# Kernel optimization log

Hardware: AMD Instinct MI355X
Metric: run time of the kernel (lower is better)

Reference implementation:

```python
import jax, jax.numpy as jnp
import numpy as np

B, T, D = 8, 1024, 1024
L = 512          # quantizer_latent_dim
V = 8192         # codebook_size
COMMIT = 0.25
PERP_COEF = 0.1


def _l2norm(v, axis=-1):
    return v * jax.lax.rsqrt(jnp.sum(v * v, axis=axis, keepdims=True) + 1e-12)


def _sq_dist(a, b):
    # ||a||^2 - 2 a.b + ||b||^2, a:[N,L] b:[V,L] -> [N,V]
    a2 = jnp.sum(a * a, axis=1, keepdims=True)
    b2 = jnp.sum(b * b, axis=1)[None, :]
    return a2 - 2.0 * jnp.einsum('nl,vl->nv', a, b) + b2


def setup_inputs() -> dict:
    key = jax.random.key(0)
    ks = jax.random.split(key, 4)
    x = jax.random.normal(ks[0], (B, T, D), dtype=jnp.float32)
    codebook = jax.random.normal(ks[1], (V, D), dtype=jnp.float32)
    W_in = jax.random.normal(ks[2], (D, L), dtype=jnp.float32) * (1.0 / np.sqrt(D))
    b_in = jnp.zeros((L,), dtype=jnp.float32)
    W_code = jax.random.normal(ks[3], (D, L), dtype=jnp.float32) * (1.0 / np.sqrt(D))
    b_code = jnp.zeros((L,), dtype=jnp.float32)
    return {"x": x, "codebook": codebook, "W_in": W_in, "b_in": b_in,
            "W_code": W_code, "b_code": b_code}


def _train_loss(quantized, x):
    e_latent = jnp.mean((jax.lax.stop_gradient(quantized) - x) ** 2) * COMMIT
    q_latent = jnp.mean((quantized - jax.lax.stop_gradient(x)) ** 2)
    return e_latent + q_latent


def reference(x, codebook, W_in, b_in, W_code, b_code):
    xf = x.reshape(-1, D)                                      # [N, D]
    latent_input = _l2norm(xf @ W_in + b_in)                   # [N, L]
    latent_code = _l2norm(codebook @ W_code + b_code)          # [V, L]
    sg_latent_code = jax.lax.stop_gradient(_l2norm(latent_code))
    distances = _sq_dist(latent_input, sg_latent_code).reshape(B, T, V)

    # approx_min_k with aggregate_to_topk (k = top_k_value = 1)
    idx = jax.lax.approx_min_k(distances, k=1, reduction_dimension=-1,
                               aggregate_to_topk=True)[1][..., 0]   # [B, T]
    encodings = jax.nn.one_hot(idx, V, dtype=x.dtype)          # [B, T, V]
    quantized = jnp.einsum('btv,vd->btd', encodings, codebook) # [B, T, D]

    codebook_usage = jnp.sum(jnp.sum(encodings, axis=(0, 1)) > 0) / V

    # train=True path: stop-grad quantized, straight-through estimator
    q_sg = jax.lax.stop_gradient(quantized)
    loss = _train_loss(q_sg, x)
    latent_quantized = q_sg @ W_code + b_code                  # code_to_latent(quantized)
    latent_x = x @ W_in + b_in                                 # input_to_latent(x)
    loss = loss + _train_loss(latent_quantized, latent_x)

    quantized_st = x + jax.lax.stop_gradient(q_sg - x)

    avg_probs = jnp.mean(encodings.reshape(-1, V), axis=0)
    log_perplexity = -jnp.sum(avg_probs * jnp.log(avg_probs + 1e-10))
    perplexity = jnp.exp(log_perplexity)
    loss = loss + PERP_COEF * log_perplexity

    return quantized_st, loss, perplexity, codebook_usage
```

## Files before the change

kernel.cpp:

```cpp
#include <hip/hip_runtime.h>
#include <hip/hip_bf16.h>
#include <stdint.h>

#define NTOK 8192
#define DDIM 1024
#define LDIM 512
#define VCB  8192
#define MROWS 16384

typedef unsigned long long u64;
typedef unsigned short ushort_t;
typedef unsigned char u8;
typedef float f32x4 __attribute__((ext_vector_type(4)));
typedef short s16x8 __attribute__((ext_vector_type(8)));

#define OFF_AB     0ull
#define OFF_QB     0ull
#define OFF_P      ((u64)MROWS * DDIM * 2)
#define OFF_QF     (OFF_P + (u64)MROWS * LDIM * 2)
#define OFF_WT     (OFF_QF + (u64)MROWS * 512)
#define OFF_B2     (OFF_WT + (u64)2 * LDIM * DDIM * 2)
#define OFF_B2B    (OFF_B2 + (u64)VCB * 4)
#define OFF_PART   (OFF_B2B + (u64)VCB * 4)
#define OFF_HIST   (OFF_PART + (u64)NTOK * 64 * 4)
#define OFF_PARTQ  (OFF_HIST + (u64)VCB * 4)
#define OFF_PARTL  (OFF_PARTQ + (u64)NTOK * 4)

__device__ __forceinline__ unsigned key_of(float f) {
  unsigned u = __float_as_uint(f);
  return (u & 0x80000000u) ? ~u : (u | 0x80000000u);
}

__device__ __forceinline__ ushort_t f2bf(float f) {
  unsigned u = __float_as_uint(f);
  unsigned r = (u + 0x7fffu + ((u >> 16) & 1u)) >> 16;
  return (ushort_t)r;
}
__device__ __forceinline__ float bf2f(unsigned b) {
  return __uint_as_float(b << 16);
}
__device__ __forceinline__ unsigned pkbf(float a, float b) {
  __hip_bfloat162 h = __float22bfloat162_rn(make_float2(a, b));
  unsigned r;
  __builtin_memcpy(&r, &h, 4);
  return r;
}

__device__ __forceinline__ void gload_lds16(const void* g, void* l) {
  __builtin_amdgcn_global_load_lds(
      (const __attribute__((address_space(1))) unsigned int*)g,
      (__attribute__((address_space(3))) unsigned int*)l, 16, 0, 0);
}

__device__ __forceinline__ f32x4 mfma16(s16x8 a, s16x8 b, f32x4 c) {
  return __builtin_amdgcn_mfma_f32_16x16x32_bf16(a, b, c, 0, 0, 0);
}
__device__ __forceinline__ f32x4 mfma8(u64 a, u64 b, f32x4 c) {
  return __builtin_amdgcn_mfma_f32_16x16x32_fp8_fp8((long long)a, (long long)b,
                                                    c, 0, 0, 0);
}

__global__ __launch_bounds__(256)
void k_wt(const float* __restrict__ Wi, const float* __restrict__ Wc,
          ushort_t* __restrict__ Wt, int* __restrict__ hist) {
  __shared__ float tile[32][33];
  const int tx = threadIdx.x, ty = threadIdx.y;
  const int t = ty * 32 + tx;
  const int lb = blockIdx.z * 512 + blockIdx.y * 32 + blockIdx.x;
  if (lb < 32) hist[lb * 256 + t] = 0;
  const float* W = blockIdx.z ? Wc : Wi;
  ushort_t* O = Wt + (blockIdx.z ? (size_t)LDIM * DDIM : 0);
  const int k0 = blockIdx.x * 32, n0 = blockIdx.y * 32;
#pragma unroll
  for (int i = 0; i < 4; ++i)
    tile[ty * 4 + i][tx] = W[(size_t)(k0 + ty * 4 + i) * LDIM + n0 + tx];
  __syncthreads();
#pragma unroll
  for (int i = 0; i < 4; ++i)
    O[(size_t)(n0 + ty * 4 + i) * DDIM + k0 + tx] = f2bf(tile[tx][ty * 4 + i]);
}

__global__ __launch_bounds__(256)
void k_cast(const float* __restrict__ x, const float* __restrict__ cb,
            ushort_t* __restrict__ Ab) {
  size_t i = ((size_t)blockIdx.x * 256 + threadIdx.x) * 8;
  const size_t half = (size_t)NTOK * DDIM;
  const float* src = (i < half) ? (x + i) : (cb + (i - half));
  float4 a = *(const float4*)src;
  float4 b = *(const float4*)(src + 4);
  uint4 o = make_uint4(pkbf(a.x, a.y), pkbf(a.z, a.w),
                       pkbf(b.x, b.y), pkbf(b.z, b.w));
  *(uint4*)&Ab[i] = o;
}

__global__ __launch_bounds__(256)
void k_latent(const ushort_t* __restrict__ Ab, const ushort_t* __restrict__ Wt,
              const float* __restrict__ bi, const float* __restrict__ bc,
              ushort_t* __restrict__ Pb) {
  __shared__ __align__(16) ushort_t As[128 * 32];
  __shared__ __align__(16) ushort_t Bs[128 * 32];
  const int t = threadIdx.x;
  const int wave = t >> 6, lane = t & 63;
  const int col0 = blockIdx.x * 128;
  const int m0 = blockIdx.y * 128;
  const bool isCode = (m0 >= NTOK);
  const u8* A = (const u8*)(Ab + (size_t)m0 * DDIM);
  const u8* W = (const u8*)(Wt + (isCode ? (size_t)LDIM * DDIM : 0) +
                            (size_t)col0 * DDIM);
  const float* bias = isCode ? bc : bi;

  const int srow = lane >> 2;
  const int rA = wave * 16 + srow;
  const int rB = 64 + wave * 16 + srow;
  const size_t goA = (size_t)rA * 2048 +
                     (((lane & 3) ^ (rA & 3) ^ ((rA >> 2) & 3)) << 4);
  const size_t goB = (size_t)rB * 2048 +
                     (((lane & 3) ^ (rB & 3) ^ ((rB >> 2) & 3)) << 4);
  u8* lwA0 = (u8*)As + (wave * 16) * 64;
  u8* lwA1 = (u8*)As + (64 + wave * 16) * 64;
  u8* lwB0 = (u8*)Bs + (wave * 16) * 64;
  u8* lwB1 = (u8*)Bs + (64 + wave * 16) * 64;

  const int wm = wave >> 1, wn = wave & 1;
  const int m = lane & 15, q = lane >> 4;
  const int pq = (q ^ (m & 3) ^ ((m >> 2) & 3)) * 16;
  int roffA[4], roffB[4];
#pragma unroll
  for (int i = 0; i < 4; ++i) {
    roffA[i] = (wm * 64 + i * 16 + m) * 64 + pq;
    roffB[i] = (wn * 64 + i * 16 + m) * 64 + pq;
  }

  f32x4 acc[4][4];
#pragma unroll
  for (int i = 0; i < 4; ++i)
#pragma unroll
    for (int j = 0; j < 4; ++j) acc[i][j] = (f32x4)(0.f);

  for (int it = 0; it < DDIM / 32; ++it) {
    const size_t kb = (size_t)it * 64;
    __syncthreads();
    gload_lds16(A + goA + kb, lwA0);
    gload_lds16(A + goB + kb, lwA1);
    gload_lds16(W + goA + kb, lwB0);
    gload_lds16(W + goB + kb, lwB1);
    __syncthreads();
    s16x8 af[4], bfr[4];
#pragma unroll
    for (int i = 0; i < 4; ++i)
      af[i] = *(const s16x8*)((const u8*)As + roffA[i]);
#pragma unroll
    for (int j = 0; j < 4; ++j)
      bfr[j] = *(const s16x8*)((const u8*)Bs + roffB[j]);
#pragma unroll
    for (int i = 0; i < 4; ++i)
#pragma unroll
      for (int j = 0; j < 4; ++j)
        acc[i][j] = mfma16(af[i], bfr[j], acc[i][j]);
  }

  float bv[4];
#pragma unroll
  for (int j = 0; j < 4; ++j) bv[j] = bias[col0 + wn * 64 + j * 16 + m];
#pragma unroll
  for (int i = 0; i < 4; ++i)
#pragma unroll
    for (int j = 0; j < 4; ++j) {
      int col = col0 + wn * 64 + j * 16 + m;
#pragma unroll
      for (int reg = 0; reg < 4; ++reg) {
        int row = m0 + wm * 64 + i * 16 + q * 4 + reg;
        Pb[(size_t)row * LDIM + col] = f2bf(acc[i][j][reg] + bv[j]);
      }
    }
}

__global__ __launch_bounds__(256)
void k_rownorm(const ushort_t* __restrict__ P, u8* __restrict__ Qf,
               ushort_t* __restrict__ Qb, float* __restrict__ b2,
               float* __restrict__ b2b) {
  const int row = blockIdx.x;
  const int t = threadIdx.x;
  const int lane = t & 63, wid = t >> 6;
  __shared__ float red[4];
  __shared__ float2 red2[4];
  __shared__ float bcast;
  const int c = t >> 5;
  const int w = (2 * t) & 63;
  const int g = w >> 4, h = w & 15;
  const int k = c * 64 + ((h < 8) ? (g * 8 + h) : (32 + g * 8 + (h - 8)));
  unsigned pv = *(const unsigned*)&P[(size_t)row * LDIM + k];
  float v0 = bf2f(pv & 0xffffu), v1 = bf2f(pv >> 16);
  float s = fmaf(v0, v0, v1 * v1);
#pragma unroll
  for (int o = 32; o > 0; o >>= 1) s += __shfl_down(s, o, 64);
  if (lane == 0) red[wid] = s;
  __syncthreads();
  if (t == 0) {
    float tot = red[0] + red[1] + red[2] + red[3];
    bcast = (float)(1.0 / sqrt((double)tot + 1e-12));
  }
  __syncthreads();
  float rs = bcast;
  int p8 = __builtin_amdgcn_cvt_pk_fp8_f32(v0 * rs, v1 * rs, 0, false);
  ((ushort_t*)Qf)[(size_t)row * 256 + t] = (ushort_t)((unsigned)p8 & 0xFFFFu);
  unsigned qp = pkbf(v0 * rs, v1 * rs);
  *(unsigned*)&Qb[(size_t)row * LDIM + k] = qp;
  if (row >= NTOK) {
    float f0 = __builtin_amdgcn_cvt_f32_fp8(p8, 0);
    float f1 = __builtin_amdgcn_cvt_f32_fp8(p8, 1);
    float g0 = bf2f(qp & 0xffffu), g1 = bf2f(qp >> 16);
    float s8 = fmaf(f0, f0, f1 * f1);
    float sb = fmaf(g0, g0, g1 * g1);
#pragma unroll
    for (int o = 32; o > 0; o >>= 1) {
      s8 += __shfl_down(s8, o, 64);
      sb += __shfl_down(sb, o, 64);
    }
    __syncthreads();
    if (lane == 0) red2[wid] = make_float2(s8, sb);
    __syncthreads();
    if (t == 0) {
      b2[row - NTOK]  = red2[0].x + red2[1].x + red2[2].x + red2[3].x;
      b2b[row - NTOK] = red2[0].y + red2[1].y + red2[2].y + red2[3].y;
    }
  }
}

__global__ __launch_bounds__(256)
void k_dist(const u8* __restrict__ Qf, const float* __restrict__ b2,
            unsigned* __restrict__ part) {
  __shared__ __align__(16) u8 S[2][128 * 64];
  u8* As = S[0];
  u8* Bs = S[1];
  const int t = threadIdx.x;
  const int wave = t >> 6, lane = t & 63;
  const int v0 = blockIdx.x * 128;
  const int n0 = blockIdx.y * 128;
  const u8* Ga = Qf + (size_t)n0 * 512;
  const u8* Gb = Qf + (size_t)(NTOK + v0) * 512;

  const int srow = lane >> 2;
  const int rA = wave * 16 + srow;
  const int rB = 64 + wave * 16 + srow;
  const size_t goA = (size_t)rA * 512 +
                     (((lane & 3) ^ (rA & 3) ^ ((rA >> 2) & 3)) << 4);
  const size_t goB = (size_t)rB * 512 +
                     (((lane & 3) ^ (rB & 3) ^ ((rB >> 2) & 3)) << 4);
  u8* lwA0 = As + (wave * 16) * 64;
  u8* lwA1 = As + (64 + wave * 16) * 64;
  u8* lwB0 = Bs + (wave * 16) * 64;
  u8* lwB1 = Bs + (64 + wave * 16) * 64;

  const int wm = wave >> 1, wn = wave & 1;
  const int m = lane & 15, q = lane >> 4;
  int roffA[4], roffB[4];
#pragma unroll
  for (int i = 0; i < 4; ++i) {
    int fr = wm * 64 + i * 16 + m;
    roffA[i] = fr * 64 + ((q ^ (fr & 3) ^ ((fr >> 2) & 3)) << 4);
    fr = wn * 64 + i * 16 + m;
    roffB[i] = fr * 64 + ((q ^ (fr & 3) ^ ((fr >> 2) & 3)) << 4);
  }

  f32x4 acc[4][4];
#pragma unroll
  for (int i = 0; i < 4; ++i)
#pragma unroll
    for (int j = 0; j < 4; ++j) acc[i][j] = (f32x4)(0.f);

  for (int it = 0; it < 8; ++it) {
    const int k0 = it * 64;
    __syncthreads();
    gload_lds16(Ga + goA + k0, lwA0);
    gload_lds16(Ga + goB + k0, lwA1);
    gload_lds16(Gb + goA + k0, lwB0);
    gload_lds16(Gb + goB + k0, lwB1);
    __syncthreads();
    ulonglong2 av[4], bv[4];
#pragma unroll
    for (int i = 0; i < 4; ++i) av[i] = *(const ulonglong2*)(As + roffA[i]);
#pragma unroll
    for (int j = 0; j < 4; ++j) bv[j] = *(const ulonglong2*)(Bs + roffB[j]);
#pragma unroll
    for (int i = 0; i < 4; ++i)
#pragma unroll
      for (int j = 0; j < 4; ++j)
        acc[i][j] = mfma8(av[i].x, bv[j].x, acc[i][j]);
#pragma unroll
    for (int i = 0; i < 4; ++i)
#pragma unroll
      for (int j = 0; j < 4; ++j)
        acc[i][j] = mfma8(av[i].y, bv[j].y, acc[i][j]);
  }

  float b2v[4];
#pragma unroll
  for (int j = 0; j < 4; ++j) b2v[j] = b2[v0 + wn * 64 + j * 16 + m];

  __syncthreads();
  unsigned* tbl = (unsigned*)S;
#pragma unroll
  for (int i = 0; i < 4; ++i)
#pragma unroll
    for (int reg = 0; reg < 4; ++reg) {
      unsigned best = 0xFFFFFFFFu;
#pragma unroll
      for (int j = 0; j < 4; ++j) {
        float key = fmaf(-2.f, acc[i][j][reg], b2v[j]);
        unsigned pk = (key_of(key) & 0xFFFFE000u) |
                      (unsigned)(v0 + wn * 64 + j * 16 + m);
        best = (pk < best) ? pk : best;
      }
      int r = wm * 64 + i * 16 + q * 4 + reg;
      int slot = (wn * 16 + m) ^ ((r & 7) << 2);
      tbl[r * 32 + slot] = best;
    }
  __syncthreads();
  if (t < 128) {
    unsigned mn = 0xFFFFFFFFu;
#pragma unroll
    for (int cc = 0; cc < 8; ++cc) {
      int gc = (cc + t) & 7;
      int base = t * 32 + ((gc * 4) ^ ((t & 7) << 2));
      uint4 v = *(const uint4*)&tbl[base];
      unsigned a = (v.x < v.y) ? v.x : v.y;
      unsigned b = (v.z < v.w) ? v.z : v.w;
      a = (a < b) ? a : b;
      mn = (a < mn) ? a : mn;
    }
    part[(size_t)(n0 + t) * 64 + blockIdx.x] = mn;
  }
}

__global__ __launch_bounds__(256)
void k_gather(const unsigned* __restrict__ part, const float* __restrict__ cb,
              const float* __restrict__ x, const ushort_t* __restrict__ P,
              const ushort_t* __restrict__ Qb, const float* __restrict__ b2b,
              float* __restrict__ out, int* __restrict__ hist,
              float* __restrict__ partq, float* __restrict__ partl) {
  const int n = blockIdx.x;
  const int t = threadIdx.x;
  const int lane = t & 63, wid = t >> 6;
  __shared__ float qin[512];
  __shared__ unsigned cand[8];
  __shared__ unsigned wcand[8];
  __shared__ int sIdx;
  __shared__ float rq[4], rl[4];

  unsigned uq = ((const unsigned*)(Qb + (size_t)n * LDIM))[t];
  qin[2 * t] = bf2f(uq & 0xffffu);
  qin[2 * t + 1] = bf2f(uq >> 16);

  if (t < 64) {
    unsigned v = part[(size_t)n * 64 + t];
#pragma unroll
    for (int it = 0; it < 8; ++it) {
      unsigned mn = v;
#pragma unroll
      for (int msk = 1; msk < 64; msk <<= 1) {
        unsigned o = (unsigned)__shfl_xor((int)mn, msk, 64);
        mn = (o < mn) ? o : mn;
      }
      if (t == 0) cand[it] = mn;
      if (v == mn) v = 0xFFFFFFFFu;
    }
  }
  __syncthreads();

  const int c = t >> 5, sl = t & 31;
  const int cidx = (int)(cand[c] & 0x1FFFu);
  const unsigned* crow =
      (const unsigned*)(Qb + (size_t)(NTOK + cidx) * LDIM) + sl * 8;
  uint4 va = *(const uint4*)(crow);
  uint4 vb = *(const uint4*)(crow + 4);
  const float* qs = &qin[sl * 16];
  float dot = 0.f;
  dot = fmaf(bf2f(va.x & 0xffffu), qs[0], dot);
  dot = fmaf(bf2f(va.x >> 16),     qs[1], dot);
  dot = fmaf(bf2f(va.y & 0xffffu), qs[2], dot);
  dot = fmaf(bf2f(va.y >> 16),     qs[3], dot);
  dot = fmaf(bf2f(va.z & 0xffffu), qs[4], dot);
  dot = fmaf(bf2f(va.z >> 16),     qs[5], dot);
  dot = fmaf(bf2f(va.w & 0xffffu), qs[6], dot);
  dot = fmaf(bf2f(va.w >> 16),     qs[7], dot);
  dot = fmaf(bf2f(vb.x & 0xffffu), qs[8], dot);
  dot = fmaf(bf2f(vb.x >> 16),     qs[9], dot);
  dot = fmaf(bf2f(vb.y & 0xffffu), qs[10], dot);
  dot = fmaf(bf2f(vb.y >> 16),     qs[11], dot);
  dot = fmaf(bf2f(vb.z & 0xffffu), qs[12], dot);
  dot = fmaf(bf2f(vb.z >> 16),     qs[13], dot);
  dot = fmaf(bf2f(vb.w & 0xffffu), qs[14], dot);
  dot = fmaf(bf2f(vb.w >> 16),     qs[15], dot);
#pragma unroll
  for (int msk = 1; msk < 32; msk <<= 1) dot += __shfl_xor(dot, msk, 32);
  if (sl == 0) {
    float key = fmaf(-2.f, dot, b2b[cidx]);
    wcand[c] = (key_of(key) & 0xFFFFE000u) | (unsigned)cidx;
  }
  __syncthreads();
  if (t == 0) {
    unsigned mm = wcand[0];
#pragma unroll
    for (int i = 1; i < 8; ++i) mm = (wcand[i] < mm) ? wcand[i] : mm;
    int iv = (int)(mm & 0x1FFFu);
    sIdx = iv;
    atomicAdd(&hist[iv], 1);
  }
  __syncthreads();
  const int iv = sIdx;

  float4 qv = *(const float4*)&cb[(size_t)iv * DDIM + t * 4];
  float4 xv = *(const float4*)&x[(size_t)n * DDIM + t * 4];
  *(float4*)&out[(size_t)n * DDIM + t * 4] = qv;
  float d0 = qv.x - xv.x, d1 = qv.y - xv.y, d2 = qv.z - xv.z, d3 = qv.w - xv.w;
  float sq = d0 * d0 + d1 * d1 + d2 * d2 + d3 * d3;
  unsigned lq = *(const unsigned*)&P[(size_t)(NTOK + iv) * LDIM + t * 2];
  unsigned lx = *(const unsigned*)&P[(size_t)n * LDIM + t * 2];
  float e0 = bf2f(lq & 0xffffu) - bf2f(lx & 0xffffu);
  float e1 = bf2f(lq >> 16) - bf2f(lx >> 16);
  float sl2 = e0 * e0 + e1 * e1;
#pragma unroll
  for (int o = 32; o > 0; o >>= 1) {
    sq += __shfl_down(sq, o, 64);
    sl2 += __shfl_down(sl2, o, 64);
  }
  if (lane == 0) { rq[wid] = sq; rl[wid] = sl2; }
  __syncthreads();
  if (t == 0) {
    partq[n] = rq[0] + rq[1] + rq[2] + rq[3];
    partl[n] = rl[0] + rl[1] + rl[2] + rl[3];
  }
}

__global__ __launch_bounds__(1024)
void k_final(const int* __restrict__ hist, const float* __restrict__ partq,
             const float* __restrict__ partl, float* __restrict__ out) {
  const int t = threadIdx.x;
  const int lane = t & 63, wid = t >> 6;
  float perp = 0.f, usedf = 0.f, sq = 0.f, sl = 0.f;
  for (int v = t; v < VCB; v += 1024) {
    int h = hist[v];
    usedf += (h > 0) ? 1.f : 0.f;
    float p = (float)h * (1.f / (float)NTOK);
    perp -= p * logf(p + 1e-10f);
  }
  for (int n = t; n < NTOK; n += 1024) {
    sq += partq[n];
    sl += partl[n];
  }
#pragma unroll
  for (int o = 32; o > 0; o >>= 1) {
    perp  += __shfl_down(perp, o, 64);
    usedf += __shfl_down(usedf, o, 64);
    sq    += __shfl_down(sq, o, 64);
    sl    += __shfl_down(sl, o, 64);
  }
  __shared__ float red[16][4];
  if (lane == 0) {
    red[wid][0] = perp; red[wid][1] = usedf; red[wid][2] = sq; red[wid][3] = sl;
  }
  __syncthreads();
  if (t == 0) {
    float Pp = 0.f, U = 0.f, SQ = 0.f, SL = 0.f;
    for (int w = 0; w < 16; ++w) {
      Pp += red[w][0]; U += red[w][1]; SQ += red[w][2]; SL += red[w][3];
    }
    float mseq = SQ / (float)((size_t)NTOK * DDIM);
    float msel = SL / (float)((size_t)NTOK * LDIM);
    float loss = 1.25f * mseq + 1.25f * msel + 0.1f * Pp;
    out[(size_t)NTOK * DDIM + 0] = loss;
    out[(size_t)NTOK * DDIM + 1] = expf(Pp);
    out[(size_t)NTOK * DDIM + 2] = U / (float)VCB;
  }
}

extern "C" void kernel_launch(void* const* d_in, const int* in_sizes, int n_in,
                              void* d_out, int out_size, void* d_ws, size_t ws_size,
                              hipStream_t stream) {
  const float* x  = (const float*)d_in[0];
  const float* cb = (const float*)d_in[1];
  const float* Wi = (const float*)d_in[2];
  const float* bi = (const float*)d_in[3];
  const float* Wc = (const float*)d_in[4];
  const float* bc = (const float*)d_in[5];
  float* out = (float*)d_out;
  char* ws = (char*)d_ws;
  ushort_t* Ab   = (ushort_t*)(ws + OFF_AB);
  ushort_t* Qb   = (ushort_t*)(ws + OFF_QB);
  ushort_t* P    = (ushort_t*)(ws + OFF_P);
  u8*       Qf   = (u8*)(ws + OFF_QF);
  ushort_t* Wt   = (ushort_t*)(ws + OFF_WT);
  float*    b2   = (float*)(ws + OFF_B2);
  float*    b2b  = (float*)(ws + OFF_B2B);
  unsigned* part = (unsigned*)(ws + OFF_PART);
  int*      hist = (int*)(ws + OFF_HIST);
  float*    partq = (float*)(ws + OFF_PARTQ);
  float*    partl = (float*)(ws + OFF_PARTL);

  hipLaunchKernelGGL(k_wt, dim3(DDIM / 32, LDIM / 32, 2), dim3(32, 8), 0,
                     stream, Wi, Wc, Wt, hist);
  hipLaunchKernelGGL(k_cast, dim3((MROWS * DDIM) / (256 * 8)), dim3(256), 0,
                     stream, x, cb, Ab);
  hipLaunchKernelGGL(k_latent, dim3(LDIM / 128, MROWS / 128), dim3(256), 0,
                     stream, Ab, Wt, bi, bc, P);
  hipLaunchKernelGGL(k_rownorm, dim3(MROWS), dim3(256), 0, stream, P, Qf, Qb,
                     b2, b2b);
  hipLaunchKernelGGL(k_dist, dim3(VCB / 128, NTOK / 128), dim3(256), 0, stream,
                     Qf, b2, part);
  hipLaunchKernelGGL(k_gather, dim3(NTOK), dim3(256), 0, stream, part, cb, x,
                     P, Qb, b2b, out, hist, partq, partl);
  hipLaunchKernelGGL(k_final, dim3(1), dim3(1024), 0, stream, hist, partq,
                     partl, out);
}
```

Baseline: 269.0 us.

## Use 32x32x64 scaled FP8 MFMA in distance kernel and wave-per-row normalization

```diff
diff --git a/kernel.cpp b/kernel.cpp
--- a/kernel.cpp
+++ b/kernel.cpp
@@ -12,7 +12,9 @@
 typedef unsigned short ushort_t;
 typedef unsigned char u8;
 typedef float f32x4 __attribute__((ext_vector_type(4)));
+typedef float f32x16 __attribute__((ext_vector_type(16)));
 typedef short s16x8 __attribute__((ext_vector_type(8)));
+typedef int i32x8 __attribute__((ext_vector_type(8)));
 
 #define OFF_AB     0ull
 #define OFF_QB     0ull
@@ -55,9 +57,13 @@
 __device__ __forceinline__ f32x4 mfma16(s16x8 a, s16x8 b, f32x4 c) {
   return __builtin_amdgcn_mfma_f32_16x16x32_bf16(a, b, c, 0, 0, 0);
 }
-__device__ __forceinline__ f32x4 mfma8(u64 a, u64 b, f32x4 c) {
-  return __builtin_amdgcn_mfma_f32_16x16x32_fp8_fp8((long long)a, (long long)b,
-                                                    c, 0, 0, 0);
+
+__device__ __forceinline__ float fp8sq4(int w) {
+  float f0 = __builtin_amdgcn_cvt_f32_fp8(w, 0);
+  float f1 = __builtin_amdgcn_cvt_f32_fp8(w, 1);
+  float f2 = __builtin_amdgcn_cvt_f32_fp8(w, 2);
+  float f3 = __builtin_amdgcn_cvt_f32_fp8(w, 3);
+  return fmaf(f0, f0, fmaf(f1, f1, fmaf(f2, f2, f3 * f3)));
 }
 
 __global__ __launch_bounds__(256)
@@ -179,50 +185,52 @@
 void k_rownorm(const ushort_t* __restrict__ P, u8* __restrict__ Qf,
                ushort_t* __restrict__ Qb, float* __restrict__ b2,
                float* __restrict__ b2b) {
-  const int row = blockIdx.x;
-  const int t = threadIdx.x;
-  const int lane = t & 63, wid = t >> 6;
-  __shared__ float red[4];
-  __shared__ float2 red2[4];
-  __shared__ float bcast;
-  const int c = t >> 5;
-  const int w = (2 * t) & 63;
-  const int g = w >> 4, h = w & 15;
-  const int k = c * 64 + ((h < 8) ? (g * 8 + h) : (32 + g * 8 + (h - 8)));
-  unsigned pv = *(const unsigned*)&P[(size_t)row * LDIM + k];
-  float v0 = bf2f(pv & 0xffffu), v1 = bf2f(pv >> 16);
-  float s = fmaf(v0, v0, v1 * v1);
-#pragma unroll
-  for (int o = 32; o > 0; o >>= 1) s += __shfl_down(s, o, 64);
-  if (lane == 0) red[wid] = s;
-  __syncthreads();
-  if (t == 0) {
-    float tot = red[0] + red[1] + red[2] + red[3];
-    bcast = (float)(1.0 / sqrt((double)tot + 1e-12));
-  }
-  __syncthreads();
-  float rs = bcast;
-  int p8 = __builtin_amdgcn_cvt_pk_fp8_f32(v0 * rs, v1 * rs, 0, false);
-  ((ushort_t*)Qf)[(size_t)row * 256 + t] = (ushort_t)((unsigned)p8 & 0xFFFFu);
-  unsigned qp = pkbf(v0 * rs, v1 * rs);
-  *(unsigned*)&Qb[(size_t)row * LDIM + k] = qp;
+  const int row = blockIdx.x * 4 + (threadIdx.x >> 6);
+  const int lane = threadIdx.x & 63;
+  uint4 u = *((const uint4*)(P + (size_t)row * LDIM) + lane);
+  float v[8];
+  v[0] = bf2f(u.x & 0xffffu); v[1] = bf2f(u.x >> 16);
+  v[2] = bf2f(u.y & 0xffffu); v[3] = bf2f(u.y >> 16);
+  v[4] = bf2f(u.z & 0xffffu); v[5] = bf2f(u.z >> 16);
+  v[6] = bf2f(u.w & 0xffffu); v[7] = bf2f(u.w >> 16);
+  float s = 0.f;
+#pragma unroll
+  for (int i = 0; i < 8; ++i) s = fmaf(v[i], v[i], s);
+#pragma unroll
+  for (int msk = 1; msk < 64; msk <<= 1) s += __shfl_xor(s, msk, 64);
+  float rs = (float)(1.0 / sqrt((double)s + 1e-12));
+  float qv[8];
+#pragma unroll
+  for (int i = 0; i < 8; ++i) qv[i] = v[i] * rs;
+  uint4 o = make_uint4(pkbf(qv[0], qv[1]), pkbf(qv[2], qv[3]),
+                       pkbf(qv[4], qv[5]), pkbf(qv[6], qv[7]));
+  *((uint4*)(Qb + (size_t)row * LDIM) + lane) = o;
+  unsigned w0 = (unsigned)__builtin_amdgcn_cvt_pk_fp8_f32(qv[0], qv[1], 0, false);
+  w0 = (unsigned)__builtin_amdgcn_cvt_pk_fp8_f32(qv[2], qv[3], (int)w0, true);
+  unsigned w1 = (unsigned)__builtin_amdgcn_cvt_pk_fp8_f32(qv[4], qv[5], 0, false);
+  w1 = (unsigned)__builtin_amdgcn_cvt_pk_fp8_f32(qv[6], qv[7], (int)w1, true);
+  const int k0 = lane * 8, c = k0 >> 6, r = k0 & 63;
+  const int p = (r < 32) ? (c * 64 + ((r >> 3) << 4))
+                         : (c * 64 + (((r - 32) >> 3) << 4) + 8);
+  *(u64*)(Qf + (size_t)row * 512 + p) = ((u64)w1 << 32) | w0;
   if (row >= NTOK) {
-    float f0 = __builtin_amdgcn_cvt_f32_fp8(p8, 0);
-    float f1 = __builtin_amdgcn_cvt_f32_fp8(p8, 1);
-    float g0 = bf2f(qp & 0xffffu), g1 = bf2f(qp >> 16);
-    float s8 = fmaf(f0, f0, f1 * f1);
-    float sb = fmaf(g0, g0, g1 * g1);
-#pragma unroll
-    for (int o = 32; o > 0; o >>= 1) {
-      s8 += __shfl_down(s8, o, 64);
-      sb += __shfl_down(sb, o, 64);
-    }
-    __syncthreads();
-    if (lane == 0) red2[wid] = make_float2(s8, sb);
-    __syncthreads();
-    if (t == 0) {
-      b2[row - NTOK]  = red2[0].x + red2[1].x + red2[2].x + red2[3].x;
-      b2b[row - NTOK] = red2[0].y + red2[1].y + red2[2].y + red2[3].y;
+    float s8 = fp8sq4((int)w0) + fp8sq4((int)w1);
+    float sb = 0.f;
+    float g[8];
+    g[0] = bf2f(o.x & 0xffffu); g[1] = bf2f(o.x >> 16);
+    g[2] = bf2f(o.y & 0xffffu); g[3] = bf2f(o.y >> 16);
+    g[4] = bf2f(o.z & 0xffffu); g[5] = bf2f(o.z >> 16);
+    g[6] = bf2f(o.w & 0xffffu); g[7] = bf2f(o.w >> 16);
+#pragma unroll
+    for (int i = 0; i < 8; ++i) sb = fmaf(g[i], g[i], sb);
+#pragma unroll
+    for (int msk = 1; msk < 64; msk <<= 1) {
+      s8 += __shfl_xor(s8, msk, 64);
+      sb += __shfl_xor(sb, msk, 64);
+    }
+    if (lane == 0) {
+      b2[row - NTOK] = s8;
+      b2b[row - NTOK] = sb;
     }
   }
 }
@@ -253,21 +261,23 @@
   u8* lwB1 = Bs + (64 + wave * 16) * 64;
 
   const int wm = wave >> 1, wn = wave & 1;
-  const int m = lane & 15, q = lane >> 4;
-  int roffA[4], roffB[4];
-#pragma unroll
-  for (int i = 0; i < 4; ++i) {
-    int fr = wm * 64 + i * 16 + m;
-    roffA[i] = fr * 64 + ((q ^ (fr & 3) ^ ((fr >> 2) & 3)) << 4);
-    fr = wn * 64 + i * 16 + m;
-    roffB[i] = fr * 64 + ((q ^ (fr & 3) ^ ((fr >> 2) & 3)) << 4);
-  }
-
-  f32x4 acc[4][4];
-#pragma unroll
-  for (int i = 0; i < 4; ++i)
-#pragma unroll
-    for (int j = 0; j < 4; ++j) acc[i][j] = (f32x4)(0.f);
+  const int c31 = lane & 31, q2 = lane >> 5;
+  int roffA[2][2], roffB[2][2];
+#pragma unroll
+  for (int ti = 0; ti < 2; ++ti) {
+    int fr = wm * 64 + ti * 32 + c31;
+    int s = (fr & 3) ^ ((fr >> 2) & 3);
+    roffA[ti][0] = fr * 64 + (((2 * q2) ^ s) << 4);
+    roffA[ti][1] = fr * 64 + (((2 * q2 + 1) ^ s) << 4);
+    fr = wn * 64 + ti * 32 + c31;
+    s = (fr & 3) ^ ((fr >> 2) & 3);
+    roffB[ti][0] = fr * 64 + (((2 * q2) ^ s) << 4);
+    roffB[ti][1] = fr * 64 + (((2 * q2 + 1) ^ s) << 4);
+  }
+
+  f32x16 acc[4];
+#pragma unroll
+  for (int i = 0; i < 4; ++i) acc[i] = (f32x16)(0.f);
 
   for (int it = 0; it < 8; ++it) {
     const int k0 = it * 64;
@@ -277,59 +287,55 @@
     gload_lds16(Gb + goA + k0, lwB0);
     gload_lds16(Gb + goB + k0, lwB1);
     __syncthreads();
-    ulonglong2 av[4], bv[4];
-#pragma unroll
-    for (int i = 0; i < 4; ++i) av[i] = *(const ulonglong2*)(As + roffA[i]);
-#pragma unroll
-    for (int j = 0; j < 4; ++j) bv[j] = *(const ulonglong2*)(Bs + roffB[j]);
-#pragma unroll
-    for (int i = 0; i < 4; ++i)
-#pragma unroll
-      for (int j = 0; j < 4; ++j)
-        acc[i][j] = mfma8(av[i].x, bv[j].x, acc[i][j]);
-#pragma unroll
-    for (int i = 0; i < 4; ++i)
-#pragma unroll
-      for (int j = 0; j < 4; ++j)
-        acc[i][j] = mfma8(av[i].y, bv[j].y, acc[i][j]);
-  }
-
-  float b2v[4];
-#pragma unroll
-  for (int j = 0; j < 4; ++j) b2v[j] = b2[v0 + wn * 64 + j * 16 + m];
-
+    i32x8 av[2], bv[2];
+#pragma unroll
+    for (int ti = 0; ti < 2; ++ti) {
+      *(uint4*)&av[ti] = *(const uint4*)(As + roffA[ti][0]);
+      *(((uint4*)&av[ti]) + 1) = *(const uint4*)(As + roffA[ti][1]);
+      *(uint4*)&bv[ti] = *(const uint4*)(Bs + roffB[ti][0]);
+      *(((uint4*)&bv[ti]) + 1) = *(const uint4*)(Bs + roffB[ti][1]);
+    }
+#pragma unroll
+    for (int ti = 0; ti < 2; ++ti)
+#pragma unroll
+      for (int tj = 0; tj < 2; ++tj)
+        acc[ti * 2 + tj] = __builtin_amdgcn_mfma_scale_f32_32x32x64_f8f6f4(
+            av[ti], bv[tj], acc[ti * 2 + tj], 0, 0, 0, 127, 0, 127);
+  }
+
+  float b2v[2];
+  int idv[2];
+#pragma unroll
+  for (int tj = 0; tj < 2; ++tj) {
+    int col = v0 + wn * 64 + tj * 32 + c31;
+    b2v[tj] = b2[col];
+    idv[tj] = col;
+  }
   __syncthreads();
   unsigned* tbl = (unsigned*)S;
 #pragma unroll
-  for (int i = 0; i < 4; ++i)
-#pragma unroll
-    for (int reg = 0; reg < 4; ++reg) {
-      unsigned best = 0xFFFFFFFFu;
-#pragma unroll
-      for (int j = 0; j < 4; ++j) {
-        float key = fmaf(-2.f, acc[i][j][reg], b2v[j]);
-        unsigned pk = (key_of(key) & 0xFFFFE000u) |
-                      (unsigned)(v0 + wn * 64 + j * 16 + m);
-        best = (pk < best) ? pk : best;
+  for (int ti = 0; ti < 2; ++ti)
+#pragma unroll
+    for (int reg = 0; reg < 16; ++reg) {
+      float kk0 = fmaf(-2.f, acc[ti * 2 + 0][reg], b2v[0]);
+      float kk1 = fmaf(-2.f, acc[ti * 2 + 1][reg], b2v[1]);
+      unsigned p0 = (key_of(kk0) & 0xFFFFE000u) | (unsigned)idv[0];
+      unsigned p1 = (key_of(kk1) & 0xFFFFE000u) | (unsigned)idv[1];
+      unsigned best = (p1 < p0) ? p1 : p0;
+#pragma unroll
+      for (int msk = 1; msk < 32; msk <<= 1) {
+        unsigned o = (unsigned)__shfl_xor((int)best, msk, 32);
+        best = (o < best) ? o : best;
       }
-      int r = wm * 64 + i * 16 + q * 4 + reg;
-      int slot = (wn * 16 + m) ^ ((r & 7) << 2);
-      tbl[r * 32 + slot] = best;
+      if (c31 == 0) {
+        int rl = wm * 64 + ti * 32 + (reg & 3) + 4 * q2 + 8 * (reg >> 2);
+        tbl[rl * 2 + wn] = best;
+      }
     }
   __syncthreads();
   if (t < 128) {
-    unsigned mn = 0xFFFFFFFFu;
-#pragma unroll
-    for (int cc = 0; cc < 8; ++cc) {
-      int gc = (cc + t) & 7;
-      int base = t * 32 + ((gc * 4) ^ ((t & 7) << 2));
-      uint4 v = *(const uint4*)&tbl[base];
-      unsigned a = (v.x < v.y) ? v.x : v.y;
-      unsigned b = (v.z < v.w) ? v.z : v.w;
-      a = (a < b) ? a : b;
-      mn = (a < mn) ? a : mn;
-    }
-    part[(size_t)(n0 + t) * 64 + blockIdx.x] = mn;
+    unsigned a = tbl[t * 2], b = tbl[t * 2 + 1];
+    part[(size_t)(n0 + t) * 64 + blockIdx.x] = (a < b) ? a : b;
   }
 }
 
@@ -504,8 +510,8 @@
                      stream, x, cb, Ab);
   hipLaunchKernelGGL(k_latent, dim3(LDIM / 128, MROWS / 128), dim3(256), 0,
                      stream, Ab, Wt, bi, bc, P);
-  hipLaunchKernelGGL(k_rownorm, dim3(MROWS), dim3(256), 0, stream, P, Qf, Qb,
-                     b2, b2b);
+  hipLaunchKernelGGL(k_rownorm, dim3(MROWS / 4), dim3(256), 0, stream, P, Qf,
+                     Qb, b2, b2b);
   hipLaunchKernelGGL(k_dist, dim3(VCB / 128, NTOK / 128), dim3(256), 0, stream,
                      Qf, b2, part);
   hipLaunchKernelGGL(k_gather, dim3(NTOK), dim3(256), 0, stream, part, cb, x,
```

Result: slower. 365.7 us (+35.9%).
